# Kernel tuning notes

Hardware: AMD Instinct MI355X
Metric: run time of the kernel (lower is better)

The kernel has to match this reference:

```python
import jax, jax.numpy as jnp
import numpy as np

TEMPERATURE = 0.1


def setup_inputs() -> dict:
    key = jax.random.key(0)
    k1, k2, k3 = jax.random.split(key, 3)
    B, C, D = 8192, 1000, 128
    features = jax.random.normal(k1, (B, D), dtype=jnp.float32)
    features = features / jnp.linalg.norm(features, axis=-1, keepdims=True)
    centers1 = jax.random.normal(k2, (C, D), dtype=jnp.float32)
    centers1 = centers1 / jnp.linalg.norm(centers1, axis=-1, keepdims=True)
    targets = jax.random.randint(k3, (B,), 0, C, dtype=jnp.int64)
    return {"centers1": centers1, "features": features, "targets": targets}


def reference(centers1, features, targets):
    B = features.shape[0]
    C = centers1.shape[0]
    dt = features.dtype

    # concatenated targets: batch targets followed by one target per class center
    t_all = jnp.concatenate([targets, jnp.arange(C, dtype=targets.dtype)])  # [B+C]
    # per-class counts over the concatenated targets (each class >= 1 from its center)
    cls_count = jnp.zeros((C,), dt).at[t_all].add(1.0)

    # positive mask [B, B+C]; zero out self-comparisons on the leading diagonal
    mask = (targets[:, None] == t_all[None, :]).astype(dt)
    logits_mask = jnp.ones((B, B + C), dt).at[jnp.arange(B), jnp.arange(B)].set(0.0)
    mask = mask * logits_mask

    feats_all = jnp.concatenate([features, centers1], axis=0)  # [B+C, D]
    logits = jnp.matmul(features, feats_all.T) / TEMPERATURE    # [B, B+C]
    logits = logits - jax.lax.stop_gradient(jnp.max(logits, axis=1, keepdims=True))

    exp_logits = jnp.exp(logits) * logits_mask
    per_ins_weight = cls_count[t_all][None, :] - mask           # [B, B+C]
    exp_logits_sum = jnp.sum(exp_logits / per_ins_weight, axis=1, keepdims=True)

    log_prob = logits - jnp.log(exp_logits_sum)
    mean_log_prob_pos = jnp.sum(mask * log_prob, axis=1) / jnp.sum(mask, axis=1)
    return -jnp.mean(mean_log_prob_pos)
```

## Files before the change

### kernel.cpp

```cpp
#include <hip/hip_runtime.h>
#include <math.h>

typedef __attribute__((ext_vector_type(8))) short short8;
typedef __attribute__((ext_vector_type(4))) float f32x4;

#define BB 8192
#define CC 1000
#define NN 9192
#define NPAD 9216
#define DD 128
#define RBW 32
#define NSPLIT 12
#define CPW 768
#define NT 48
#define K2F 14.426950408889634f

#define WS_CLS   0
#define WS_TCOL  1024
#define WS_RCP0  10240
#define WS_RCP1  19456
#define WS_SPART 28672
#define WS_PPART 126976
#define WS_F2    225280
#define WS_BS    815104

static __device__ __forceinline__ unsigned short f2bf(float x) {
    unsigned int b = __float_as_uint(x);
    unsigned int r = (b + 0x7FFFu + ((b >> 16) & 1u)) >> 16;
    return (unsigned short)r;
}
static __device__ __forceinline__ float fexp2(float x) {
    float r; asm("v_exp_f32 %0, %1" : "=v"(r) : "v"(x)); return r;
}
static __device__ __forceinline__ float flog2(float x) {
    float r; asm("v_log_f32 %0, %1" : "=v"(r) : "v"(x)); return r;
}

__global__ __launch_bounds__(1024) void prep_kernel(
    const float* __restrict__ feats, const float* __restrict__ ctrs,
    const int* __restrict__ tgt, unsigned short* __restrict__ F2,
    int* __restrict__ cls, int* __restrict__ tcol,
    float* __restrict__ rcp0, float* __restrict__ rcp1)
{
    const int tid = threadIdx.x;
    if (blockIdx.x < 144) {
        int u = blockIdx.x * 1024 + tid;
        int j = u >> 4, quad = u & 15;
        int k0 = quad * 8;
        float4 v0 = {0.f,0.f,0.f,0.f}, v1 = {0.f,0.f,0.f,0.f};
        if (j < BB) {
            v0 = *(const float4*)&feats[(size_t)j * DD + k0];
            v1 = *(const float4*)&feats[(size_t)j * DD + k0 + 4];
        } else if (j < NN) {
            v0 = *(const float4*)&ctrs[(size_t)(j - BB) * DD + k0];
            v1 = *(const float4*)&ctrs[(size_t)(j - BB) * DD + k0 + 4];
        }
        short8 o;
        o[0]=f2bf(v0.x); o[1]=f2bf(v0.y); o[2]=f2bf(v0.z); o[3]=f2bf(v0.w);
        o[4]=f2bf(v1.x); o[5]=f2bf(v1.y); o[6]=f2bf(v1.z); o[7]=f2bf(v1.w);
        size_t offb = (size_t)((((j >> 4) * 4 + (quad >> 2)) * 64 + (quad & 3) * 16 + (j & 15)) * 8);
        *(short8*)&F2[offb] = o;
        return;
    }

    __shared__ int h[1024];
    h[tid] = 0;
    __syncthreads();
    for (int i = tid; i < BB; i += 1024) atomicAdd(&h[tgt[i]], 1);
    __syncthreads();

    cls[tid] = h[tid];

    for (int j = tid; j < NPAD; j += 1024) {
        if (j < NN) {
            int c = (j < BB) ? tgt[j] : (j - BB);
            int n = h[c] + 1;
            tcol[j] = c;
            rcp0[j] = 1.0f / (float)n;
            rcp1[j] = (n > 1) ? 1.0f / (float)(n - 1) : 0.0f;
        } else { tcol[j] = -2; rcp0[j] = 0.0f; rcp1[j] = 0.0f; }
    }
}

static __device__ __forceinline__ void loadB(const unsigned short* __restrict__ F2,
                                             int j0, int lane8, short8 (&buf)[4]) {
#pragma unroll
    for (int ks = 0; ks < 4; ++ks)
        buf[ks] = *(const short8*)&F2[(size_t)(((j0 >> 4) * 4 + ks) * 512 + lane8)];
}

static __device__ __forceinline__ void mfma8(const short8 (&af)[4][2], const short8 (&b)[4],
                                             f32x4 (&acc)[2]) {
    const f32x4 z4 = {0.f, 0.f, 0.f, 0.f};
#pragma unroll
    for (int fm = 0; fm < 2; ++fm)
        acc[fm] = __builtin_amdgcn_mfma_f32_16x16x32_bf16(af[0][fm], b[0], z4, 0, 0, 0);
#pragma unroll
    for (int ks = 1; ks < 4; ++ks)
#pragma unroll
        for (int fm = 0; fm < 2; ++fm)
            acc[fm] = __builtin_amdgcn_mfma_f32_16x16x32_bf16(
                af[ks][fm], b[ks], acc[fm], 0, 0, 0);
}

template<bool DIAG>
static __device__ __forceinline__ void epi8(const f32x4 (&acc)[2], float r0, float r1,
                                            int tj, int j0, int l15, int rowbase,
                                            const int (&ti)[8],
                                            float (&Sl)[8], float (&Pl)[8]) {
    const int col = j0 + l15;
#pragma unroll
    for (int fm = 0; fm < 2; ++fm)
#pragma unroll
        for (int q = 0; q < 4; ++q) {
            const int x = fm * 4 + q;
            float d = acc[fm][q];
            float l2 = fmaf(d, K2F, -K2F);
            float e = fexp2(l2);
            bool m = (tj == ti[x]);
            if (DIAG) {
                bool self = (col == rowbase + fm * 16 + q);
                if (self) { e = 0.f; m = false; }
            }
            float rw = m ? r1 : r0;
            Sl[x] = fmaf(e, rw, Sl[x]);
            Pl[x] += m ? d : 0.f;
        }
}

__global__ __launch_bounds__(256, 3) void main_kernel(
    const unsigned short* __restrict__ F2, const int* __restrict__ tcol,
    const float* __restrict__ rcp0, const float* __restrict__ rcp1,
    float* __restrict__ S_part, float* __restrict__ P_part)
{
    const int tid  = threadIdx.x;
    const int lane = tid & 63;
    const int wave = tid >> 6;
    const int l15 = lane & 15, l4 = lane >> 4;
    const int lane8 = lane * 8;
    const int row0 = blockIdx.x * (4 * RBW) + wave * RBW;
    const int split = blockIdx.y;
    const int cb = split * CPW;
    const int rowbase = row0 + l4 * 4;

    short8 af[4][2];
#pragma unroll
    for (int fm = 0; fm < 2; ++fm)
#pragma unroll
        for (int ks = 0; ks < 4; ++ks)
            af[ks][fm] = *(const short8*)&F2[(size_t)((((row0 >> 4) + fm) * 4 + ks) * 512 + lane8)];

    int ti[8];
#pragma unroll
    for (int fm = 0; fm < 2; ++fm)
#pragma unroll
        for (int q = 0; q < 4; ++q)
            ti[fm * 4 + q] = tcol[rowbase + fm * 16 + q];

    float Sl[8], Pl[8];
#pragma unroll
    for (int x = 0; x < 8; ++x) { Sl[x] = 0.f; Pl[x] = 0.f; }

    short8 b0[4], b1[4], b2[4];
    float r0A, r0B, r0C, r1A, r1B, r1C;
    int tjA, tjB, tjC;
    loadB(F2, cb, lane8, b0);
    r0A = rcp0[cb + l15]; r1A = rcp1[cb + l15]; tjA = tcol[cb + l15];
    loadB(F2, cb + 16, lane8, b1);
    r0B = rcp0[cb + 16 + l15]; r1B = rcp1[cb + 16 + l15]; tjB = tcol[cb + 16 + l15];

#pragma unroll 1
    for (int tt = 0; tt < NT; tt += 3) {
        {
            if (tt + 2 < NT) {
                int j = cb + (tt + 2) * 16;
                loadB(F2, j, lane8, b2);
                r0C = rcp0[j + l15]; r1C = rcp1[j + l15]; tjC = tcol[j + l15];
            }
            const int j0 = cb + tt * 16;
            f32x4 acc[2];
            mfma8(af, b0, acc);
            if ((unsigned)(j0 - row0) < 32u)
                epi8<true >(acc, r0A, r1A, tjA, j0, l15, rowbase, ti, Sl, Pl);
            else
                epi8<false>(acc, r0A, r1A, tjA, j0, l15, rowbase, ti, Sl, Pl);
        }
        {
            if (tt + 3 < NT) {
                int j = cb + (tt + 3) * 16;
                loadB(F2, j, lane8, b0);
                r0A = rcp0[j + l15]; r1A = rcp1[j + l15]; tjA = tcol[j + l15];
            }
            const int j0 = cb + (tt + 1) * 16;
            f32x4 acc[2];
            mfma8(af, b1, acc);
            if ((unsigned)(j0 - row0) < 32u)
                epi8<true >(acc, r0B, r1B, tjB, j0, l15, rowbase, ti, Sl, Pl);
            else
                epi8<false>(acc, r0B, r1B, tjB, j0, l15, rowbase, ti, Sl, Pl);
        }
        {
            if (tt + 4 < NT) {
                int j = cb + (tt + 4) * 16;
                loadB(F2, j, lane8, b1);
                r0B = rcp0[j + l15]; r1B = rcp1[j + l15]; tjB = tcol[j + l15];
            }
            const int j0 = cb + (tt + 2) * 16;
            f32x4 acc[2];
            mfma8(af, b2, acc);
            if ((unsigned)(j0 - row0) < 32u)
                epi8<true >(acc, r0C, r1C, tjC, j0, l15, rowbase, ti, Sl, Pl);
            else
                epi8<false>(acc, r0C, r1C, tjC, j0, l15, rowbase, ti, Sl, Pl);
        }
    }

#pragma unroll
    for (int idx = 0; idx < 8; ++idx) {
        float S = Sl[idx], P = Pl[idx];
#pragma unroll
        for (int off = 1; off < 16; off <<= 1) {
            S += __shfl_xor(S, off, 64);
            P += __shfl_xor(P, off, 64);
        }
        if (l15 == 0) {
            int row = row0 + (idx >> 2) * 16 + l4 * 4 + (idx & 3);
            S_part[(size_t)row * NSPLIT + split] = S;
            P_part[(size_t)row * NSPLIT + split] = P;
        }
    }
}

__global__ __launch_bounds__(256) void final1_kernel(
    const int* __restrict__ tgt, const int* __restrict__ cls,
    const float* __restrict__ S_part, const float* __restrict__ P_part,
    float* __restrict__ bs)
{
    const int tid = threadIdx.x;
    const int i = blockIdx.x * 256 + tid;
    float S = 0.f, P = 0.f;
    const float4* sp = (const float4*)&S_part[(size_t)i * NSPLIT];
    const float4* pp = (const float4*)&P_part[(size_t)i * NSPLIT];
#pragma unroll
    for (int q = 0; q < NSPLIT / 4; ++q) {
        float4 a = sp[q]; S += (a.x + a.y) + (a.z + a.w);
        float4 b = pp[q]; P += (b.x + b.y) + (b.z + b.w);
    }
    const float npos = (float)cls[tgt[i]];
    float lp = fmaf(K2F, P / npos, -K2F) - flog2(S);

#pragma unroll
    for (int off = 1; off < 64; off <<= 1) lp += __shfl_xor(lp, off, 64);
    __shared__ float wsum[4];
    if ((tid & 63) == 0) wsum[tid >> 6] = lp;
    __syncthreads();
    if (tid == 0) bs[blockIdx.x] = wsum[0] + wsum[1] + wsum[2] + wsum[3];
}

__global__ void final2_kernel(const float* __restrict__ bs, float* __restrict__ out) {
    const int t = threadIdx.x;
    float v = (t < 32) ? bs[t] : 0.f;
#pragma unroll
    for (int off = 1; off < 64; off <<= 1) v += __shfl_xor(v, off, 64);
    if (t == 0) out[0] = -0.6931471805599453f * (v / (float)BB);
}

extern "C" void kernel_launch(void* const* d_in, const int* in_sizes, int n_in,
                              void* d_out, int out_size, void* d_ws, size_t ws_size,
                              hipStream_t stream) {
    const float* ctrs  = (const float*)d_in[0];
    const float* feats = (const float*)d_in[1];
    const int*   tgt   = (const int*)d_in[2];
    float* out = (float*)d_out;
    float* ws  = (float*)d_ws;

    int*   cls  = (int*)(ws + WS_CLS);
    int*   tcol = (int*)(ws + WS_TCOL);
    float* rcp0 = ws + WS_RCP0;
    float* rcp1 = ws + WS_RCP1;
    float* Sp   = ws + WS_SPART;
    float* Pp   = ws + WS_PPART;
    float* bs   = ws + WS_BS;
    unsigned short* F2 = (unsigned short*)(ws + WS_F2);

    prep_kernel<<<dim3(145), dim3(1024), 0, stream>>>(feats, ctrs, tgt, F2, cls, tcol, rcp0, rcp1);
    main_kernel<<<dim3(BB / (4 * RBW), NSPLIT), dim3(256), 0, stream>>>(F2, tcol, rcp0, rcp1, Sp, Pp);
    final1_kernel<<<dim3(BB / 256), dim3(256), 0, stream>>>(tgt, cls, Sp, Pp, bs);
    final2_kernel<<<dim3(1), dim3(64), 0, stream>>>(bs, out);
}
```

Measured before the change: 45.20 us.

## Widen column tile to 32, pack per-column metadata into float4, fewer splits

The main loop now processes 32 columns per step (2x2 MFMA tiles per wave) with double buffering instead of 16 columns with triple buffering. Per-column target, rcp0 and rcp1 are packed into a single float4 array so each column needs one load instead of three. The column split count drops from 12 to 8, giving fewer partial sums and a 64-block by 8 grid. Launch bounds go from 3 to 2 waves per SIMD to make room for the larger register footprint, which cuts occupancy and leaves 512 blocks to spread over the GPU.

```diff
diff --git a/kernel.cpp b/kernel.cpp
--- a/kernel.cpp
+++ b/kernel.cpp
@@ -10,19 +10,17 @@
 #define NPAD 9216
 #define DD 128
 #define RBW 32
-#define NSPLIT 12
-#define CPW 768
-#define NT 48
+#define NSPLIT 8
+#define CPB 1152
+#define NT 36
 #define K2F 14.426950408889634f
 
 #define WS_CLS   0
-#define WS_TCOL  1024
-#define WS_RCP0  10240
-#define WS_RCP1  19456
-#define WS_SPART 28672
-#define WS_PPART 126976
-#define WS_F2    225280
-#define WS_BS    815104
+#define WS_META  1024
+#define WS_SPART 37888
+#define WS_PPART 103424
+#define WS_F2    168960
+#define WS_BS    463872
 
 static __device__ __forceinline__ unsigned short f2bf(float x) {
     unsigned int b = __float_as_uint(x);
@@ -39,8 +37,7 @@
 __global__ __launch_bounds__(1024) void prep_kernel(
     const float* __restrict__ feats, const float* __restrict__ ctrs,
     const int* __restrict__ tgt, unsigned short* __restrict__ F2,
-    int* __restrict__ cls, int* __restrict__ tcol,
-    float* __restrict__ rcp0, float* __restrict__ rcp1)
+    int* __restrict__ cls, float4* __restrict__ meta)
 {
     const int tid = threadIdx.x;
     if (blockIdx.x < 144) {
@@ -72,65 +69,77 @@
     cls[tid] = h[tid];
 
     for (int j = tid; j < NPAD; j += 1024) {
+        float4 m = {__int_as_float(-2), 0.f, 0.f, 0.f};
         if (j < NN) {
             int c = (j < BB) ? tgt[j] : (j - BB);
             int n = h[c] + 1;
-            tcol[j] = c;
-            rcp0[j] = 1.0f / (float)n;
-            rcp1[j] = (n > 1) ? 1.0f / (float)(n - 1) : 0.0f;
-        } else { tcol[j] = -2; rcp0[j] = 0.0f; rcp1[j] = 0.0f; }
-    }
-}
-
-static __device__ __forceinline__ void loadB(const unsigned short* __restrict__ F2,
-                                             int j0, int lane8, short8 (&buf)[4]) {
-#pragma unroll
-    for (int ks = 0; ks < 4; ++ks)
-        buf[ks] = *(const short8*)&F2[(size_t)(((j0 >> 4) * 4 + ks) * 512 + lane8)];
-}
-
-static __device__ __forceinline__ void mfma8(const short8 (&af)[4][2], const short8 (&b)[4],
-                                             f32x4 (&acc)[2]) {
+            m.x = __int_as_float(c);
+            m.y = 1.0f / (float)n;
+            m.z = (n > 1) ? 1.0f / (float)(n - 1) : 0.0f;
+        }
+        meta[j] = m;
+    }
+}
+
+static __device__ __forceinline__ void loadB32(const unsigned short* __restrict__ F2,
+                                               int j0, int lane8, short8 (&buf)[8]) {
+#pragma unroll
+    for (int fn = 0; fn < 2; ++fn)
+#pragma unroll
+        for (int ks = 0; ks < 4; ++ks)
+            buf[fn * 4 + ks] = *(const short8*)&F2[(size_t)(((((j0 >> 4) + fn) * 4 + ks) * 512) + lane8)];
+}
+
+static __device__ __forceinline__ void mfma32(const short8 (&af)[4][2], const short8 (&b)[8],
+                                              f32x4 (&acc)[2][2]) {
     const f32x4 z4 = {0.f, 0.f, 0.f, 0.f};
 #pragma unroll
     for (int fm = 0; fm < 2; ++fm)
-        acc[fm] = __builtin_amdgcn_mfma_f32_16x16x32_bf16(af[0][fm], b[0], z4, 0, 0, 0);
+#pragma unroll
+        for (int fn = 0; fn < 2; ++fn)
+            acc[fm][fn] = __builtin_amdgcn_mfma_f32_16x16x32_bf16(af[0][fm], b[fn * 4], z4, 0, 0, 0);
 #pragma unroll
     for (int ks = 1; ks < 4; ++ks)
 #pragma unroll
         for (int fm = 0; fm < 2; ++fm)
-            acc[fm] = __builtin_amdgcn_mfma_f32_16x16x32_bf16(
-                af[ks][fm], b[ks], acc[fm], 0, 0, 0);
+#pragma unroll
+            for (int fn = 0; fn < 2; ++fn)
+                acc[fm][fn] = __builtin_amdgcn_mfma_f32_16x16x32_bf16(
+                    af[ks][fm], b[fn * 4 + ks], acc[fm][fn], 0, 0, 0);
 }
 
 template<bool DIAG>
-static __device__ __forceinline__ void epi8(const f32x4 (&acc)[2], float r0, float r1,
-                                            int tj, int j0, int l15, int rowbase,
-                                            const int (&ti)[8],
-                                            float (&Sl)[8], float (&Pl)[8]) {
-    const int col = j0 + l15;
-#pragma unroll
-    for (int fm = 0; fm < 2; ++fm)
-#pragma unroll
-        for (int q = 0; q < 4; ++q) {
-            const int x = fm * 4 + q;
-            float d = acc[fm][q];
-            float l2 = fmaf(d, K2F, -K2F);
-            float e = fexp2(l2);
-            bool m = (tj == ti[x]);
-            if (DIAG) {
-                bool self = (col == rowbase + fm * 16 + q);
-                if (self) { e = 0.f; m = false; }
+static __device__ __forceinline__ void epi32(const f32x4 (&acc)[2][2], const float4 (&mt)[2],
+                                             int j0, int l15, int rowbase,
+                                             const int (&ti)[8],
+                                             float (&Sl)[8], float (&Pl)[8]) {
+#pragma unroll
+    for (int fn = 0; fn < 2; ++fn) {
+        const int tj = __float_as_int(mt[fn].x);
+        const float r0 = mt[fn].y, r1 = mt[fn].z;
+        const int col = j0 + fn * 16 + l15;
+#pragma unroll
+        for (int fm = 0; fm < 2; ++fm)
+#pragma unroll
+            for (int q = 0; q < 4; ++q) {
+                const int x = fm * 4 + q;
+                float d = acc[fm][fn][q];
+                float l2 = fmaf(d, K2F, -K2F);
+                float e = fexp2(l2);
+                bool m = (tj == ti[x]);
+                if (DIAG) {
+                    bool self = (col == rowbase + fm * 16 + q);
+                    if (self) { e = 0.f; m = false; }
+                }
+                float rw = m ? r1 : r0;
+                Sl[x] = fmaf(e, rw, Sl[x]);
+                Pl[x] += m ? d : 0.f;
             }
-            float rw = m ? r1 : r0;
-            Sl[x] = fmaf(e, rw, Sl[x]);
-            Pl[x] += m ? d : 0.f;
-        }
-}
-
-__global__ __launch_bounds__(256, 3) void main_kernel(
-    const unsigned short* __restrict__ F2, const int* __restrict__ tcol,
-    const float* __restrict__ rcp0, const float* __restrict__ rcp1,
+    }
+}
+
+__global__ __launch_bounds__(256, 2) void main_kernel(
+    const unsigned short* __restrict__ F2, const float4* __restrict__ meta,
     float* __restrict__ S_part, float* __restrict__ P_part)
 {
     const int tid  = threadIdx.x;
@@ -140,7 +149,7 @@
     const int lane8 = lane * 8;
     const int row0 = blockIdx.x * (4 * RBW) + wave * RBW;
     const int split = blockIdx.y;
-    const int cb = split * CPW;
+    const int cb = split * CPB;
     const int rowbase = row0 + l4 * 4;
 
     short8 af[4][2];
@@ -155,63 +164,42 @@
     for (int fm = 0; fm < 2; ++fm)
 #pragma unroll
         for (int q = 0; q < 4; ++q)
-            ti[fm * 4 + q] = tcol[rowbase + fm * 16 + q];
+            ti[fm * 4 + q] = __float_as_int(meta[rowbase + fm * 16 + q].x);
 
     float Sl[8], Pl[8];
 #pragma unroll
     for (int x = 0; x < 8; ++x) { Sl[x] = 0.f; Pl[x] = 0.f; }
 
-    short8 b0[4], b1[4], b2[4];
-    float r0A, r0B, r0C, r1A, r1B, r1C;
-    int tjA, tjB, tjC;
-    loadB(F2, cb, lane8, b0);
-    r0A = rcp0[cb + l15]; r1A = rcp1[cb + l15]; tjA = tcol[cb + l15];
-    loadB(F2, cb + 16, lane8, b1);
-    r0B = rcp0[cb + 16 + l15]; r1B = rcp1[cb + 16 + l15]; tjB = tcol[cb + 16 + l15];
+    short8 bA[8], bB[8];
+    float4 mA[2], mB[2];
+    loadB32(F2, cb, lane8, bA);
+    mA[0] = meta[cb + l15]; mA[1] = meta[cb + 16 + l15];
 
 #pragma unroll 1
-    for (int tt = 0; tt < NT; tt += 3) {
+    for (int tt = 0; tt < NT; tt += 2) {
+        {
+            if (tt + 1 < NT) {
+                int j = cb + (tt + 1) * 32;
+                loadB32(F2, j, lane8, bB);
+                mB[0] = meta[j + l15]; mB[1] = meta[j + 16 + l15];
+            }
+            const int j0 = cb + tt * 32;
+            f32x4 acc[2][2];
+            mfma32(af, bA, acc);
+            if (j0 == row0) epi32<true >(acc, mA, j0, l15, rowbase, ti, Sl, Pl);
+            else            epi32<false>(acc, mA, j0, l15, rowbase, ti, Sl, Pl);
+        }
         {
             if (tt + 2 < NT) {
-                int j = cb + (tt + 2) * 16;
-                loadB(F2, j, lane8, b2);
-                r0C = rcp0[j + l15]; r1C = rcp1[j + l15]; tjC = tcol[j + l15];
+                int j = cb + (tt + 2) * 32;
+                loadB32(F2, j, lane8, bA);
+                mA[0] = meta[j + l15]; mA[1] = meta[j + 16 + l15];
             }
-            const int j0 = cb + tt * 16;
-            f32x4 acc[2];
-            mfma8(af, b0, acc);
-            if ((unsigned)(j0 - row0) < 32u)
-                epi8<true >(acc, r0A, r1A, tjA, j0, l15, rowbase, ti, Sl, Pl);
-            else
-                epi8<false>(acc, r0A, r1A, tjA, j0, l15, rowbase, ti, Sl, Pl);
-        }
-        {
-            if (tt + 3 < NT) {
-                int j = cb + (tt + 3) * 16;
-                loadB(F2, j, lane8, b0);
-                r0A = rcp0[j + l15]; r1A = rcp1[j + l15]; tjA = tcol[j + l15];
-            }
-            const int j0 = cb + (tt + 1) * 16;
-            f32x4 acc[2];
-            mfma8(af, b1, acc);
-            if ((unsigned)(j0 - row0) < 32u)
-                epi8<true >(acc, r0B, r1B, tjB, j0, l15, rowbase, ti, Sl, Pl);
-            else
-                epi8<false>(acc, r0B, r1B, tjB, j0, l15, rowbase, ti, Sl, Pl);
-        }
-        {
-            if (tt + 4 < NT) {
-                int j = cb + (tt + 4) * 16;
-                loadB(F2, j, lane8, b1);
-                r0B = rcp0[j + l15]; r1B = rcp1[j + l15]; tjB = tcol[j + l15];
-            }
-            const int j0 = cb + (tt + 2) * 16;
-            f32x4 acc[2];
-            mfma8(af, b2, acc);
-            if ((unsigned)(j0 - row0) < 32u)
-                epi8<true >(acc, r0C, r1C, tjC, j0, l15, rowbase, ti, Sl, Pl);
-            else
-                epi8<false>(acc, r0C, r1C, tjC, j0, l15, rowbase, ti, Sl, Pl);
+            const int j0 = cb + (tt + 1) * 32;
+            f32x4 acc[2][2];
+            mfma32(af, bB, acc);
+            if (j0 == row0) epi32<true >(acc, mB, j0, l15, rowbase, ti, Sl, Pl);
+            else            epi32<false>(acc, mB, j0, l15, rowbase, ti, Sl, Pl);
         }
     }
 
@@ -274,17 +262,15 @@
     float* out = (float*)d_out;
     float* ws  = (float*)d_ws;
 
-    int*   cls  = (int*)(ws + WS_CLS);
-    int*   tcol = (int*)(ws + WS_TCOL);
-    float* rcp0 = ws + WS_RCP0;
-    float* rcp1 = ws + WS_RCP1;
-    float* Sp   = ws + WS_SPART;
-    float* Pp   = ws + WS_PPART;
-    float* bs   = ws + WS_BS;
+    int*    cls  = (int*)(ws + WS_CLS);
+    float4* meta = (float4*)(ws + WS_META);
+    float*  Sp   = ws + WS_SPART;
+    float*  Pp   = ws + WS_PPART;
+    float*  bs   = ws + WS_BS;
     unsigned short* F2 = (unsigned short*)(ws + WS_F2);
 
-    prep_kernel<<<dim3(145), dim3(1024), 0, stream>>>(feats, ctrs, tgt, F2, cls, tcol, rcp0, rcp1);
-    main_kernel<<<dim3(BB / (4 * RBW), NSPLIT), dim3(256), 0, stream>>>(F2, tcol, rcp0, rcp1, Sp, Pp);
+    prep_kernel<<<dim3(145), dim3(1024), 0, stream>>>(feats, ctrs, tgt, F2, cls, meta);
+    main_kernel<<<dim3(BB / (4 * RBW), NSPLIT), dim3(256), 0, stream>>>(F2, meta, Sp, Pp);
     final1_kernel<<<dim3(BB / 256), dim3(256), 0, stream>>>(tgt, cls, Sp, Pp, bs);
     final2_kernel<<<dim3(1), dim3(64), 0, stream>>>(bs, out);
 }
```

Result: no change. 45.43 us (+0.5%).
